# Kernel tuning notes

Hardware: AMD Instinct MI355X
Metric: run time of the kernel (lower is better)

## Reference

```python
import jax, jax.numpy as jnp
import numpy as np


def _bilinear(x, py, px):
    # x: [B,C,H,W]; py,px: [B,K,Ho,Wo] fractional sample coords (zero pad outside)
    B, C, H, W = x.shape
    K, Ho, Wo = py.shape[1], py.shape[2], py.shape[3]
    xf = x.reshape(B, C, H * W)
    y0 = jnp.floor(py)
    x0 = jnp.floor(px)

    def gather(yi, xi):
        valid = (yi >= 0) & (yi <= H - 1) & (xi >= 0) & (xi <= W - 1)
        yc = jnp.clip(yi, 0, H - 1).astype(jnp.int32)
        xc = jnp.clip(xi, 0, W - 1).astype(jnp.int32)
        idx = (yc * W + xc).reshape(B, 1, -1)  # [B,1,K*Ho*Wo]
        v = jnp.take_along_axis(xf, idx, axis=2)  # [B,C,K*Ho*Wo]
        return v * valid.reshape(B, 1, -1)

    wy1 = (py - y0).reshape(B, 1, -1)
    wx1 = (px - x0).reshape(B, 1, -1)
    wy0 = 1.0 - wy1
    wx0 = 1.0 - wx1
    v = (gather(y0, x0) * (wy0 * wx0)
         + gather(y0, x0 + 1) * (wy0 * wx1)
         + gather(y0 + 1, x0) * (wy1 * wx0)
         + gather(y0 + 1, x0 + 1) * (wy1 * wx1))
    return v.reshape(B, C, K, Ho, Wo)


def _deform_merge(x, w_off, b_off, w_def, gamma, beta):
    B, C, H, W = x.shape
    Co = w_def.shape[0]
    K, stride = 4, 2  # 2x2 kernel
    Ho, Wo = H // 2, W // 2
    # offset-predicting conv (same k/s/p as deform conv): [B, 2K, Ho, Wo]
    off = jax.lax.conv_general_dilated(x, w_off, (stride, stride), 'VALID')
    off = off + b_off[None, :, None, None]
    off = off.reshape(B, K, 2, Ho, Wo)  # (dy, dx) per kernel tap
    ky = jnp.arange(K) // 2
    kx = jnp.arange(K) % 2
    base_y = (jnp.arange(Ho) * stride)[None, None, :, None] + ky[None, :, None, None]
    base_x = (jnp.arange(Wo) * stride)[None, None, None, :] + kx[None, :, None, None]
    py = base_y.astype(x.dtype) + off[:, :, 0]
    px = base_x.astype(x.dtype) + off[:, :, 1]
    sampled = _bilinear(x, py, px)  # [B,C,K,Ho,Wo]
    y = jnp.einsum('bckhw,ock->bohw', sampled, w_def.reshape(Co, C, K))
    # BatchNorm2d (training-mode batch stats, eps=1e-5) + exact GELU
    mu = y.mean(axis=(0, 2, 3), keepdims=True)
    var = y.var(axis=(0, 2, 3), keepdims=True)
    yn = (y - mu) * jax.lax.rsqrt(var + 1e-5)
    yn = yn * gamma[None, :, None, None] + beta[None, :, None, None]
    yg = jax.nn.gelu(yn, approximate=False)
    return yg.reshape(B, Co, Ho * Wo).transpose(0, 2, 1)  # [B, L/4, Co]


def setup_inputs() -> dict:
    key = jax.random.key(0)
    k0, k1, k2 = jax.random.split(key, 3)
    B, C, H, W, Co = 16, 96, 112, 112, 192
    x = jax.random.normal(k0, (B, C, H, W), jnp.float32)
    # conv_offset: 2*kh*kw = 8 output channels (zero-init in mmcv; small random here)
    w_off = jax.random.normal(k1, (8, C, 2, 2), jnp.float32) * 0.01
    b_off = jnp.zeros((8,), jnp.float32)
    w_def = jax.random.normal(k2, (Co, C, 2, 2), jnp.float32) * (1.0 / np.sqrt(C * 4))
    gamma = jnp.ones((Co,), jnp.float32)
    beta = jnp.zeros((Co,), jnp.float32)
    return {"x": x, "h": H, "w": W, "w_off": w_off, "b_off": b_off,
            "w_def": w_def, "gamma": gamma, "beta": beta}


def reference(x, h, w, w_off, b_off, w_def, gamma, beta):
    assert x.shape[2] == h and x.shape[3] == w
    return _deform_merge(x, w_off, b_off, w_def, gamma, beta)
```

## Files before the change

### kernel.cpp

```cpp
#include <hip/hip_runtime.h>
#include <math.h>

#define BB 16
#define CC 96
#define HH 112
#define WW 112
#define HO 56
#define WO 56
#define LL (HO*WO)
#define CO 192
#define CKD 384
#define NPIX (BB*LL)

#define TPX 28
#define CHK 8
#define NCHUNK 12
#define WROWS 4
#define WCOLS 64
#define WSTRIDE 260
#define APAD 40

#define WS_SSUM  16
#define WS_SSQS  208
#define WS_B_OFF 4096
#define B_ELEMS  73728

typedef short bf16x8 __attribute__((ext_vector_type(8)));
typedef float f32x4  __attribute__((ext_vector_type(4)));

__device__ __forceinline__ void split8(const float4 a0, const float4 a1,
                                       bf16x8& hi, bf16x8& lo)
{
    float f[8] = {a0.x, a0.y, a0.z, a0.w, a1.x, a1.y, a1.z, a1.w};
    #pragma unroll
    for (int j = 0; j < 8; ++j) {
        unsigned bits = __float_as_uint(f[j]);
        float fh = __uint_as_float(bits & 0xFFFF0000u);
        float fl = f[j] - fh;
        hi[j] = (short)(bits >> 16);
        lo[j] = (short)(__float_as_uint(fl) >> 16);
    }
}

__global__ void k_zero(float* __restrict__ ws) {
    int t = threadIdx.x;
    if (t < 384) ws[WS_SSUM + t] = 0.f;
}

__global__ void k_prep(const float* __restrict__ w_def,
                       unsigned short* __restrict__ bhi,
                       unsigned short* __restrict__ blo,
                       float* __restrict__ ws)
{
    if (blockIdx.x == 0 && threadIdx.x < 384) ws[WS_SSUM + threadIdx.x] = 0.f;
    int t = blockIdx.x * 256 + threadIdx.x;
    if (t >= 12 * 12 * 64) return;
    int ln  = t & 63;
    int ks  = (t >> 6) % 12;
    int ntg = t / (64 * 12);
    int n  = ntg * 16 + (ln & 15);
    int k0 = ks * 32 + (ln >> 4) * 8;
    const float* wp = w_def + (size_t)n * CKD + k0;
    #pragma unroll
    for (int j = 0; j < 8; ++j) {
        float f = wp[j];
        unsigned bits = __float_as_uint(f);
        float fh = __uint_as_float(bits & 0xFFFF0000u);
        float fl = f - fh;
        bhi[t * 8 + j] = (unsigned short)(bits >> 16);
        blo[t * 8 + j] = (unsigned short)(__float_as_uint(fl) >> 16);
    }
}

template<bool PREP>
__device__ __forceinline__ void tile_body(
    const float* __restrict__ x, const float* __restrict__ w_off,
    const float* __restrict__ b_off, const float* __restrict__ w_def,
    const unsigned short* __restrict__ bhi, const unsigned short* __restrict__ blo,
    float* win, unsigned short* smAh, unsigned short* smAl, float* soff,
    int b, int bx, int tid, f32x4 (&acc)[2][3])
{
    const int oy  = bx >> 1;
    const int ox0 = (bx & 1) * TPX;
    const int iy  = oy * 2;
    const int ix0 = ox0 * 2;
    const int ln = tid & 63;
    const int w  = tid >> 6;

    float dacc = 0.f;
    const int cpix = tid >> 3;
    const int coch = tid & 7;
    const int spair = tid / 14;
    const int sq    = tid % 14;
    for (int ch = 0; ch < NCHUNK; ++ch) {
        __syncthreads();
        if (tid < 224) {
            int c = spair >> 1, r = spair & 1;
            const float* src = x + (((size_t)(b * CC + ch * CHK + c) * HH) + iy + r) * WW + ix0 + sq * 4;
            *(float4*)&win[(c * 2 + r) * 56 + sq * 4] = *(const float4*)src;
        }
        __syncthreads();
        if (tid < 224) {
            const float* wb = w_off + (size_t)coch * (CC * 4) + ch * CHK * 4;
            #pragma unroll
            for (int c = 0; c < CHK; ++c) {
                float2 t0 = *(const float2*)&win[(c * 2 + 0) * 56 + 2 * cpix];
                float2 t1 = *(const float2*)&win[(c * 2 + 1) * 56 + 2 * cpix];
                float4 a = *(const float4*)(wb + c * 4);
                dacc += t0.x * a.x + t0.y * a.y + t1.x * a.z + t1.y * a.w;
            }
        }
    }
    if (tid < 224) soff[cpix * 8 + coch] = dacc + b_off[coch];

    const int row0 = ln & 15;
    const int kg   = ln >> 4;
    const int skk = tid & 31;
    const int sc  = skk >> 2;
    const int sk  = skk & 3;
    const int sky = sk >> 1, skx = sk & 1;
    const int wr0 = iy - 1, wc0 = ix0 - 4;

    for (int ch = NCHUNK - 1; ch >= 0; --ch) {
        __syncthreads();
        #pragma unroll
        for (int j = 0; j < 2; ++j) {
            int li = tid + 256 * j;
            int cg = li & 15;
            int pr = li >> 4;
            int r = pr & 3, c = pr >> 2;
            int gr = min(max(wr0 + r, 0), HH - 1);
            int gc0 = wc0 + cg * 4;
            const float* src = x + (((size_t)(b * CC + ch * CHK + c) * HH) + gr) * WW;
            float4 v;
            if (gc0 >= 0 && gc0 <= WW - 4) {
                v = *(const float4*)(src + gc0);
            } else {
                v.x = src[min(max(gc0 + 0, 0), WW - 1)];
                v.y = src[min(max(gc0 + 1, 0), WW - 1)];
                v.z = src[min(max(gc0 + 2, 0), WW - 1)];
                v.w = src[min(max(gc0 + 3, 0), WW - 1)];
            }
            *(float4*)&win[c * WSTRIDE + r * WCOLS + cg * 4] = v;
        }
        __syncthreads();
        {
            const float* xc = x + ((size_t)(b * CC + ch * CHK + sc) * HH) * WW;
            const float* wchan = &win[sc * WSTRIDE];
            #pragma unroll
            for (int j = 0; j < 4; ++j) {
                if (j < 3 || tid < 128) {
                    int pix = (tid >> 5) + 8 * j;
                    float2 so = *(const float2*)&soff[pix * 8 + 2 * sk];
                    float fy = (float)(iy + sky) + so.x;
                    float fx = (float)(ix0 + 2 * pix + skx) + so.y;
                    float y0f = floorf(fy), x0f = floorf(fx);
                    int y0 = (int)y0f, x0 = (int)x0f;
                    float wy1 = fy - y0f, wx1 = fx - x0f;
                    float wy0 = 1.f - wy1, wx0 = 1.f - wx1;
                    int y1 = y0 + 1, x1 = x0 + 1;
                    bool vy0 = (y0 >= 0) && (y0 <= HH - 1);
                    bool vy1 = (y1 >= 0) && (y1 <= HH - 1);
                    bool vx0 = (x0 >= 0) && (x0 <= WW - 1);
                    bool vx1 = (x1 >= 0) && (x1 <= WW - 1);
                    int cy0 = min(max(y0, 0), HH - 1), cy1 = min(max(y1, 0), HH - 1);
                    int cx0 = min(max(x0, 0), WW - 1), cx1 = min(max(x1, 0), WW - 1);
                    float w00 = (vy0 && vx0) ? wy0 * wx0 : 0.f;
                    float w01 = (vy0 && vx1) ? wy0 * wx1 : 0.f;
                    float w10 = (vy1 && vx0) ? wy1 * wx0 : 0.f;
                    float w11 = (vy1 && vx1) ? wy1 * wx1 : 0.f;
                    int ry0 = cy0 - wr0, ry1 = cy1 - wr0;
                    int rx0 = cx0 - wc0, rx1 = cx1 - wc0;
                    bool inw = ((unsigned)ry0 <= (unsigned)(WROWS - 1)) &&
                               ((unsigned)ry1 <= (unsigned)(WROWS - 1)) &&
                               ((unsigned)rx0 <= (unsigned)(WCOLS - 1)) &&
                               ((unsigned)rx1 <= (unsigned)(WCOLS - 1));
                    float v;
                    if (inw) {
                        v = w00 * wchan[ry0 * WCOLS + rx0] + w01 * wchan[ry0 * WCOLS + rx1]
                          + w10 * wchan[ry1 * WCOLS + rx0] + w11 * wchan[ry1 * WCOLS + rx1];
                    } else {
                        v = w00 * xc[cy0 * WW + cx0] + w01 * xc[cy0 * WW + cx1]
                          + w10 * xc[cy1 * WW + cx0] + w11 * xc[cy1 * WW + cx1];
                    }
                    unsigned u = __float_as_uint(v);
                    float fh = __uint_as_float(u & 0xFFFF0000u);
                    smAh[pix * APAD + skk] = (unsigned short)(u >> 16);
                    smAl[pix * APAD + skk] = (unsigned short)(__float_as_uint(v - fh) >> 16);
                }
            }
        }
        __syncthreads();
        bf16x8 ah[2], al[2];
        #pragma unroll
        for (int mt = 0; mt < 2; ++mt) {
            ah[mt] = *(const bf16x8*)&smAh[(mt * 16 + row0) * APAD + kg * 8];
            al[mt] = *(const bf16x8*)&smAl[(mt * 16 + row0) * APAD + kg * 8];
        }
        #pragma unroll
        for (int nt = 0; nt < 3; ++nt) {
            bf16x8 bh, bl;
            if (PREP) {
                size_t idx = ((size_t)(((w * 3 + nt) * 12 + ch) * 64) + ln) * 8;
                bh = *(const bf16x8*)(bhi + idx);
                bl = *(const bf16x8*)(blo + idx);
            } else {
                const float* wp = w_def + (size_t)(w * 48 + nt * 16 + row0) * CKD
                                + ch * 32 + kg * 8;
                float4 b0 = *(const float4*)wp;
                float4 b1 = *(const float4*)(wp + 4);
                split8(b0, b1, bh, bl);
            }
            #pragma unroll
            for (int mt = 0; mt < 2; ++mt) {
                acc[mt][nt] = __builtin_amdgcn_mfma_f32_16x16x32_bf16(ah[mt], bh, acc[mt][nt], 0, 0, 0);
                acc[mt][nt] = __builtin_amdgcn_mfma_f32_16x16x32_bf16(ah[mt], bl, acc[mt][nt], 0, 0, 0);
                acc[mt][nt] = __builtin_amdgcn_mfma_f32_16x16x32_bf16(al[mt], bh, acc[mt][nt], 0, 0, 0);
            }
        }
    }
}

template<bool PREP>
__global__ __launch_bounds__(256, 6) void k_main(
    const float* __restrict__ x, const float* __restrict__ w_off,
    const float* __restrict__ b_off, const float* __restrict__ w_def,
    const unsigned short* __restrict__ bhi, const unsigned short* __restrict__ blo,
    float* __restrict__ yout, float* __restrict__ ws)
{
    __shared__ float win[CHK * WSTRIDE];
    __shared__ unsigned short smAh[32 * APAD];
    __shared__ unsigned short smAl[32 * APAD];
    __shared__ float soff[TPX * 8];

    const int tid = threadIdx.x;
    const int b  = blockIdx.y;
    const int bx = blockIdx.x;
    const int ln = tid & 63;
    const int w  = tid >> 6;
    const int row0 = ln & 15;
    const int kg   = ln >> 4;

    if (tid < 128) {
        int rr = 28 + (tid >> 5), cc = tid & 31;
        smAh[rr * APAD + cc] = 0;
        smAl[rr * APAD + cc] = 0;
    }

    f32x4 acc[2][3];
    #pragma unroll
    for (int mt = 0; mt < 2; ++mt)
        #pragma unroll
        for (int nt = 0; nt < 3; ++nt)
            acc[mt][nt] = (f32x4){0.f, 0.f, 0.f, 0.f};

    tile_body<PREP>(x, w_off, b_off, w_def, bhi, blo,
                    win, smAh, smAl, soff, b, bx, tid, acc);

    #pragma unroll
    for (int nt = 0; nt < 3; ++nt) {
        float s = 0.f, q = 0.f;
        #pragma unroll
        for (int mt = 0; mt < 2; ++mt)
            #pragma unroll
            for (int r = 0; r < 4; ++r) {
                float v = acc[mt][nt][r];
                s += v; q += v * v;
            }
        s += __shfl_xor(s, 16); s += __shfl_xor(s, 32);
        q += __shfl_xor(q, 16); q += __shfl_xor(q, 32);
        if (ln < 16) {
            atomicAdd(&ws[WS_SSUM + w * 48 + nt * 16 + ln], s);
            atomicAdd(&ws[WS_SSQS + w * 48 + nt * 16 + ln], q);
        }
    }
    int oy = bx >> 1, ox0 = (bx & 1) * TPX;
    size_t obase = (size_t)b * LL + (size_t)oy * WO + ox0;
    #pragma unroll
    for (int mt = 0; mt < 2; ++mt)
        #pragma unroll
        for (int r = 0; r < 4; ++r) {
            int pp = mt * 16 + kg * 4 + r;
            if (pp < TPX) {
                float* dst = yout + (obase + pp) * CO + w * 48 + row0;
                dst[0]  = acc[mt][0][r];
                dst[16] = acc[mt][1][r];
                dst[32] = acc[mt][2][r];
            }
        }
}

__global__ __launch_bounds__(256) void k_bn_gelu(
    float* __restrict__ out,
    const float* __restrict__ gamma,
    const float* __restrict__ beta,
    const float* __restrict__ ws)
{
    __shared__ float ssc[CO], ssh[CO];
    int t = threadIdx.x;
    if (t < CO) {
        float n = (float)NPIX;
        float mu = ws[WS_SSUM + t] / n;
        float var = ws[WS_SSQS + t] / n - mu * mu;
        float sc = gamma[t] * rsqrtf(fmaxf(var, 0.f) + 1e-5f);
        ssc[t] = sc;
        ssh[t] = beta[t] - mu * sc;
    }
    __syncthreads();
    long long i4 = ((long long)blockIdx.x * 256 + t) * 4;
    if (i4 >= (long long)NPIX * CO) return;
    int o0 = (int)(i4 % CO);
    float4* p = (float4*)(out + i4);
    float4 v = *p;
    float f[4] = { v.x, v.y, v.z, v.w };
    #pragma unroll
    for (int j = 0; j < 4; ++j) {
        float z = ssc[o0 + j] * f[j] + ssh[o0 + j];
        f[j] = 0.5f * z * (1.f + erff(z * 0.70710678118654752f));
    }
    v.x = f[0]; v.y = f[1]; v.z = f[2]; v.w = f[3];
    *p = v;
}

extern "C" void kernel_launch(void* const* d_in, const int* in_sizes, int n_in,
                              void* d_out, int out_size, void* d_ws, size_t ws_size,
                              hipStream_t stream)
{
    const float *x = nullptr, *w_off = nullptr, *b_off = nullptr;
    const float *w_def = nullptr, *gamma = nullptr, *beta = nullptr;
    for (int i = 0; i < n_in; ++i) {
        int s = in_sizes[i];
        if      (s == 19267584) x     = (const float*)d_in[i];
        else if (s == 3072)     w_off = (const float*)d_in[i];
        else if (s == 8)        b_off = (const float*)d_in[i];
        else if (s == 73728)    w_def = (const float*)d_in[i];
        else if (s == 192) { if (!gamma) gamma = (const float*)d_in[i];
                             else        beta  = (const float*)d_in[i]; }
    }
    if (!x || !w_off || !b_off || !w_def || !gamma || !beta) {
        x = (const float*)d_in[0]; w_off = (const float*)d_in[3];
        b_off = (const float*)d_in[4]; w_def = (const float*)d_in[5];
        gamma = (const float*)d_in[6]; beta = (const float*)d_in[7];
    }

    float* ws = (float*)d_ws;
    float* out = (float*)d_out;

    unsigned short* bhi = (unsigned short*)((char*)d_ws + WS_B_OFF);
    unsigned short* blo = bhi + B_ELEMS;
    bool prep = ws_size >= (size_t)(WS_B_OFF + 2 * B_ELEMS * sizeof(unsigned short));

    if (prep) {
        k_prep<<<36, 256, 0, stream>>>(w_def, bhi, blo, ws);
        k_main<true><<<dim3(112, BB), 256, 0, stream>>>(x, w_off, b_off, w_def, bhi, blo, out, ws);
    } else {
        k_zero<<<1, 384, 0, stream>>>(ws);
        k_main<false><<<dim3(112, BB), 256, 0, stream>>>(x, w_off, b_off, w_def, bhi, blo, out, ws);
    }
    k_bn_gelu<<<dim3((int)(((long long)NPIX*CO/4 + 255) / 256)), 256, 0, stream>>>(out, gamma, beta, ws);
}
```

Measured before the change: 368.5 us.

## Split offset conv into own kernel and use 512-thread main tiles

Moves the offset-predicting conv into a separate kernel that writes per-pixel offsets to workspace, computed per full output row. The main kernel then loads those offsets and runs with 512 threads, each wave owning one 16-row M tile, so staging and sampling work is spread over twice as many threads. This removes the serialized offset prologue from each main block and raises parallelism. In exchange it adds a launch and an offset round trip through global memory, and it depends on a larger workspace; the old path remains as a fallback and its occupancy hint was changed.

Result: faster. 336.5 us (-8.7%).

```diff
diff --git a/kernel.cpp b/kernel.cpp
--- a/kernel.cpp
+++ b/kernel.cpp
@@ -19,11 +19,14 @@
 #define WCOLS 64
 #define WSTRIDE 260
 #define APAD 40
+#define OSTRIDE 228
 
 #define WS_SSUM  16
 #define WS_SSQS  208
 #define WS_B_OFF 4096
 #define B_ELEMS  73728
+#define WS_SOFF_OFF 299008
+#define SOFF_BYTES (BB*HO*WO*8*4)
 
 typedef short bf16x8 __attribute__((ext_vector_type(8)));
 typedef float f32x4  __attribute__((ext_vector_type(4)));
@@ -72,66 +75,96 @@
     }
 }
 
-template<bool PREP>
-__device__ __forceinline__ void tile_body(
+__global__ __launch_bounds__(512) void k_off(
     const float* __restrict__ x, const float* __restrict__ w_off,
-    const float* __restrict__ b_off, const float* __restrict__ w_def,
+    const float* __restrict__ b_off, float* __restrict__ soff_all)
+{
+    __shared__ float win[CHK * OSTRIDE];
+    const int t  = threadIdx.x;
+    const int oy = blockIdx.x;
+    const int b  = blockIdx.y;
+    const int iy = oy * 2;
+    const int pix = t >> 3, och = t & 7;
+    float dacc = 0.f;
+    for (int ch = 0; ch < NCHUNK; ++ch) {
+        __syncthreads();
+        if (t < 448) {
+            int c = t / 56, u = t % 56;
+            int r = u / 28, q = u % 28;
+            const float* src = x + (((size_t)(b*CC + ch*CHK + c)*HH) + iy + r)*WW + q*4;
+            *(float4*)&win[c*OSTRIDE + r*112 + q*4] = *(const float4*)src;
+        }
+        __syncthreads();
+        if (t < 448) {
+            const float* wb = w_off + (size_t)och * (CC*4) + ch*CHK*4;
+            #pragma unroll
+            for (int c = 0; c < CHK; ++c) {
+                float2 t0 = *(const float2*)&win[c*OSTRIDE + 2*pix];
+                float2 t1 = *(const float2*)&win[c*OSTRIDE + 112 + 2*pix];
+                float4 a = *(const float4*)(wb + c*4);
+                dacc += t0.x*a.x + t0.y*a.y + t1.x*a.z + t1.y*a.w;
+            }
+        }
+    }
+    if (t < 448)
+        soff_all[((size_t)(b*HO + oy)*WO)*8 + t] = dacc + b_off[och];
+}
+
+__global__ __launch_bounds__(512, 8) void k_main8(
+    const float* __restrict__ x,
     const unsigned short* __restrict__ bhi, const unsigned short* __restrict__ blo,
-    float* win, unsigned short* smAh, unsigned short* smAl, float* soff,
-    int b, int bx, int tid, f32x4 (&acc)[2][3])
-{
+    const float* __restrict__ soff_all,
+    float* __restrict__ yout, float* __restrict__ ws)
+{
+    __shared__ float win[CHK * WSTRIDE];
+    __shared__ unsigned short smAh[32 * APAD];
+    __shared__ unsigned short smAl[32 * APAD];
+    __shared__ float soff[TPX * 8];
+
+    const int tid = threadIdx.x;
+    const int b  = blockIdx.y;
+    const int bx = blockIdx.x;
     const int oy  = bx >> 1;
     const int ox0 = (bx & 1) * TPX;
     const int iy  = oy * 2;
     const int ix0 = ox0 * 2;
     const int ln = tid & 63;
     const int w  = tid >> 6;
-
-    float dacc = 0.f;
-    const int cpix = tid >> 3;
-    const int coch = tid & 7;
-    const int spair = tid / 14;
-    const int sq    = tid % 14;
-    for (int ch = 0; ch < NCHUNK; ++ch) {
-        __syncthreads();
-        if (tid < 224) {
-            int c = spair >> 1, r = spair & 1;
-            const float* src = x + (((size_t)(b * CC + ch * CHK + c) * HH) + iy + r) * WW + ix0 + sq * 4;
-            *(float4*)&win[(c * 2 + r) * 56 + sq * 4] = *(const float4*)src;
-        }
-        __syncthreads();
-        if (tid < 224) {
-            const float* wb = w_off + (size_t)coch * (CC * 4) + ch * CHK * 4;
-            #pragma unroll
-            for (int c = 0; c < CHK; ++c) {
-                float2 t0 = *(const float2*)&win[(c * 2 + 0) * 56 + 2 * cpix];
-                float2 t1 = *(const float2*)&win[(c * 2 + 1) * 56 + 2 * cpix];
-                float4 a = *(const float4*)(wb + c * 4);
-                dacc += t0.x * a.x + t0.y * a.y + t1.x * a.z + t1.y * a.w;
-            }
-        }
-    }
-    if (tid < 224) soff[cpix * 8 + coch] = dacc + b_off[coch];
-
+    const int wr = w & 1;
+    const int wc = w >> 1;
     const int row0 = ln & 15;
     const int kg   = ln >> 4;
+
+    if (tid < 128) {
+        int rr = 28 + (tid >> 5), cc = tid & 31;
+        smAh[rr*APAD + cc] = 0;
+        smAl[rr*APAD + cc] = 0;
+    }
+    if (tid < 56) {
+        const float* sp = soff_all + ((size_t)(b*HO + oy)*WO + ox0)*8;
+        *(float4*)&soff[tid*4] = *(const float4*)(sp + tid*4);
+    }
+
+    const int cg  = tid & 15;
+    const int pr  = tid >> 4;
+    const int sr  = pr & 3;
+    const int scn = pr >> 2;
     const int skk = tid & 31;
     const int sc  = skk >> 2;
     const int sk  = skk & 3;
     const int sky = sk >> 1, skx = sk & 1;
     const int wr0 = iy - 1, wc0 = ix0 - 4;
 
+    f32x4 acc[3];
+    #pragma unroll
+    for (int nt = 0; nt < 3; ++nt) acc[nt] = (f32x4){0.f, 0.f, 0.f, 0.f};
+
     for (int ch = NCHUNK - 1; ch >= 0; --ch) {
         __syncthreads();
-        #pragma unroll
-        for (int j = 0; j < 2; ++j) {
-            int li = tid + 256 * j;
-            int cg = li & 15;
-            int pr = li >> 4;
-            int r = pr & 3, c = pr >> 2;
-            int gr = min(max(wr0 + r, 0), HH - 1);
+        {
+            int gr = min(max(wr0 + sr, 0), HH - 1);
             int gc0 = wc0 + cg * 4;
-            const float* src = x + (((size_t)(b * CC + ch * CHK + c) * HH) + gr) * WW;
+            const float* src = x + (((size_t)(b*CC + ch*CHK + scn)*HH) + gr)*WW;
             float4 v;
             if (gc0 >= 0 && gc0 <= WW - 4) {
                 v = *(const float4*)(src + gc0);
@@ -141,19 +174,19 @@
                 v.z = src[min(max(gc0 + 2, 0), WW - 1)];
                 v.w = src[min(max(gc0 + 3, 0), WW - 1)];
             }
-            *(float4*)&win[c * WSTRIDE + r * WCOLS + cg * 4] = v;
+            *(float4*)&win[scn*WSTRIDE + sr*WCOLS + cg*4] = v;
         }
         __syncthreads();
         {
-            const float* xc = x + ((size_t)(b * CC + ch * CHK + sc) * HH) * WW;
-            const float* wchan = &win[sc * WSTRIDE];
+            const float* xc = x + ((size_t)(b*CC + ch*CHK + sc)*HH)*WW;
+            const float* wchan = &win[sc*WSTRIDE];
             #pragma unroll
-            for (int j = 0; j < 4; ++j) {
-                if (j < 3 || tid < 128) {
-                    int pix = (tid >> 5) + 8 * j;
-                    float2 so = *(const float2*)&soff[pix * 8 + 2 * sk];
+            for (int j = 0; j < 2; ++j) {
+                int pix = (tid >> 5) + 16 * j;
+                if (pix < TPX) {
+                    float2 so = *(const float2*)&soff[pix*8 + 2*sk];
                     float fy = (float)(iy + sky) + so.x;
-                    float fx = (float)(ix0 + 2 * pix + skx) + so.y;
+                    float fx = (float)(ix0 + 2*pix + skx) + so.y;
                     float y0f = floorf(fy), x0f = floorf(fx);
                     int y0 = (int)y0f, x0 = (int)x0f;
                     float wy1 = fy - y0f, wx1 = fx - x0f;
@@ -177,36 +210,195 @@
                                ((unsigned)rx1 <= (unsigned)(WCOLS - 1));
                     float v;
                     if (inw) {
-                        v = w00 * wchan[ry0 * WCOLS + rx0] + w01 * wchan[ry0 * WCOLS + rx1]
-                          + w10 * wchan[ry1 * WCOLS + rx0] + w11 * wchan[ry1 * WCOLS + rx1];
+                        v = w00 * wchan[ry0*WCOLS + rx0] + w01 * wchan[ry0*WCOLS + rx1]
+                          + w10 * wchan[ry1*WCOLS + rx0] + w11 * wchan[ry1*WCOLS + rx1];
                     } else {
-                        v = w00 * xc[cy0 * WW + cx0] + w01 * xc[cy0 * WW + cx1]
-                          + w10 * xc[cy1 * WW + cx0] + w11 * xc[cy1 * WW + cx1];
+                        v = w00 * xc[cy0*WW + cx0] + w01 * xc[cy0*WW + cx1]
+                          + w10 * xc[cy1*WW + cx0] + w11 * xc[cy1*WW + cx1];
                     }
                     unsigned u = __float_as_uint(v);
                     float fh = __uint_as_float(u & 0xFFFF0000u);
-                    smAh[pix * APAD + skk] = (unsigned short)(u >> 16);
-                    smAl[pix * APAD + skk] = (unsigned short)(__float_as_uint(v - fh) >> 16);
+                    smAh[pix*APAD + skk] = (unsigned short)(u >> 16);
+                    smAl[pix*APAD + skk] = (unsigned short)(__float_as_uint(v - fh) >> 16);
                 }
             }
         }
         __syncthreads();
+        bf16x8 ah = *(const bf16x8*)&smAh[(wr*16 + row0)*APAD + kg*8];
+        bf16x8 al = *(const bf16x8*)&smAl[(wr*16 + row0)*APAD + kg*8];
+        #pragma unroll
+        for (int nt = 0; nt < 3; ++nt) {
+            size_t idx = ((size_t)(((wc*3 + nt)*12 + ch)*64) + ln)*8;
+            bf16x8 bh = *(const bf16x8*)(bhi + idx);
+            bf16x8 bl = *(const bf16x8*)(blo + idx);
+            acc[nt] = __builtin_amdgcn_mfma_f32_16x16x32_bf16(ah, bh, acc[nt], 0, 0, 0);
+            acc[nt] = __builtin_amdgcn_mfma_f32_16x16x32_bf16(ah, bl, acc[nt], 0, 0, 0);
+            acc[nt] = __builtin_amdgcn_mfma_f32_16x16x32_bf16(al, bh, acc[nt], 0, 0, 0);
+        }
+    }
+
+    #pragma unroll
+    for (int nt = 0; nt < 3; ++nt) {
+        float s = 0.f, q = 0.f;
+        #pragma unroll
+        for (int r = 0; r < 4; ++r) {
+            float v = acc[nt][r];
+            s += v; q += v * v;
+        }
+        s += __shfl_xor(s, 16); s += __shfl_xor(s, 32);
+        q += __shfl_xor(q, 16); q += __shfl_xor(q, 32);
+        if (ln < 16) {
+            atomicAdd(&ws[WS_SSUM + wc*48 + nt*16 + ln], s);
+            atomicAdd(&ws[WS_SSQS + wc*48 + nt*16 + ln], q);
+        }
+    }
+    size_t obase = (size_t)b * LL + (size_t)oy * WO + ox0;
+    #pragma unroll
+    for (int r = 0; r < 4; ++r) {
+        int pp = wr*16 + kg*4 + r;
+        if (pp < TPX) {
+            float* dst = yout + (obase + pp)*CO + wc*48 + row0;
+            dst[0]  = acc[0][r];
+            dst[16] = acc[1][r];
+            dst[32] = acc[2][r];
+        }
+    }
+}
+
+template<bool PREP>
+__device__ __forceinline__ void tile_body(
+    const float* __restrict__ x, const float* __restrict__ w_off,
+    const float* __restrict__ b_off, const float* __restrict__ w_def,
+    const unsigned short* __restrict__ bhi, const unsigned short* __restrict__ blo,
+    float* win, unsigned short* smAh, unsigned short* smAl, float* soff,
+    int b, int bx, int tid, f32x4 (&acc)[2][3])
+{
+    const int oy  = bx >> 1;
+    const int ox0 = (bx & 1) * TPX;
+    const int iy  = oy * 2;
+    const int ix0 = ox0 * 2;
+    const int ln = tid & 63;
+    const int w  = tid >> 6;
+
+    float dacc = 0.f;
+    const int cpix = tid >> 3;
+    const int coch = tid & 7;
+    const int spair = tid / 14;
+    const int sq    = tid % 14;
+    for (int ch = 0; ch < NCHUNK; ++ch) {
+        __syncthreads();
+        if (tid < 224) {
+            int c = spair >> 1, r = spair & 1;
+            const float* src = x + (((size_t)(b*CC + ch*CHK + c)*HH) + iy + r)*WW + ix0 + sq*4;
+            *(float4*)&win[(c*2 + r)*56 + sq*4] = *(const float4*)src;
+        }
+        __syncthreads();
+        if (tid < 224) {
+            const float* wb = w_off + (size_t)coch*(CC*4) + ch*CHK*4;
+            #pragma unroll
+            for (int c = 0; c < CHK; ++c) {
+                float2 t0 = *(const float2*)&win[(c*2 + 0)*56 + 2*cpix];
+                float2 t1 = *(const float2*)&win[(c*2 + 1)*56 + 2*cpix];
+                float4 a = *(const float4*)(wb + c*4);
+                dacc += t0.x*a.x + t0.y*a.y + t1.x*a.z + t1.y*a.w;
+            }
+        }
+    }
+    if (tid < 224) soff[cpix*8 + coch] = dacc + b_off[coch];
+
+    const int row0 = ln & 15;
+    const int kg   = ln >> 4;
+    const int skk = tid & 31;
+    const int sc  = skk >> 2;
+    const int sk  = skk & 3;
+    const int sky = sk >> 1, skx = sk & 1;
+    const int wr0 = iy - 1, wc0 = ix0 - 4;
+
+    for (int ch = NCHUNK - 1; ch >= 0; --ch) {
+        __syncthreads();
+        #pragma unroll
+        for (int j = 0; j < 2; ++j) {
+            int li = tid + 256*j;
+            int cg = li & 15;
+            int pr = li >> 4;
+            int r = pr & 3, c = pr >> 2;
+            int gr = min(max(wr0 + r, 0), HH - 1);
+            int gc0 = wc0 + cg*4;
+            const float* src = x + (((size_t)(b*CC + ch*CHK + c)*HH) + gr)*WW;
+            float4 v;
+            if (gc0 >= 0 && gc0 <= WW - 4) {
+                v = *(const float4*)(src + gc0);
+            } else {
+                v.x = src[min(max(gc0 + 0, 0), WW - 1)];
+                v.y = src[min(max(gc0 + 1, 0), WW - 1)];
+                v.z = src[min(max(gc0 + 2, 0), WW - 1)];
+                v.w = src[min(max(gc0 + 3, 0), WW - 1)];
+            }
+            *(float4*)&win[c*WSTRIDE + r*WCOLS + cg*4] = v;
+        }
+        __syncthreads();
+        {
+            const float* xc = x + ((size_t)(b*CC + ch*CHK + sc)*HH)*WW;
+            const float* wchan = &win[sc*WSTRIDE];
+            #pragma unroll
+            for (int j = 0; j < 4; ++j) {
+                if (j < 3 || tid < 128) {
+                    int pix = (tid >> 5) + 8*j;
+                    float2 so = *(const float2*)&soff[pix*8 + 2*sk];
+                    float fy = (float)(iy + sky) + so.x;
+                    float fx = (float)(ix0 + 2*pix + skx) + so.y;
+                    float y0f = floorf(fy), x0f = floorf(fx);
+                    int y0 = (int)y0f, x0 = (int)x0f;
+                    float wy1 = fy - y0f, wx1 = fx - x0f;
+                    float wy0 = 1.f - wy1, wx0 = 1.f - wx1;
+                    int y1 = y0 + 1, x1 = x0 + 1;
+                    bool vy0 = (y0 >= 0) && (y0 <= HH - 1);
+                    bool vy1 = (y1 >= 0) && (y1 <= HH - 1);
+                    bool vx0 = (x0 >= 0) && (x0 <= WW - 1);
+                    bool vx1 = (x1 >= 0) && (x1 <= WW - 1);
+                    int cy0 = min(max(y0, 0), HH - 1), cy1 = min(max(y1, 0), HH - 1);
+                    int cx0 = min(max(x0, 0), WW - 1), cx1 = min(max(x1, 0), WW - 1);
+                    float w00 = (vy0 && vx0) ? wy0*wx0 : 0.f;
+                    float w01 = (vy0 && vx1) ? wy0*wx1 : 0.f;
+                    float w10 = (vy1 && vx0) ? wy1*wx0 : 0.f;
+                    float w11 = (vy1 && vx1) ? wy1*wx1 : 0.f;
+                    int ry0 = cy0 - wr0, ry1 = cy1 - wr0;
+                    int rx0 = cx0 - wc0, rx1 = cx1 - wc0;
+                    bool inw = ((unsigned)ry0 <= (unsigned)(WROWS - 1)) &&
+                               ((unsigned)ry1 <= (unsigned)(WROWS - 1)) &&
+                               ((unsigned)rx0 <= (unsigned)(WCOLS - 1)) &&
+                               ((unsigned)rx1 <= (unsigned)(WCOLS - 1));
+                    float v;
+                    if (inw) {
+                        v = w00*wchan[ry0*WCOLS + rx0] + w01*wchan[ry0*WCOLS + rx1]
+                          + w10*wchan[ry1*WCOLS + rx0] + w11*wchan[ry1*WCOLS + rx1];
+                    } else {
+                        v = w00*xc[cy0*WW + cx0] + w01*xc[cy0*WW + cx1]
+                          + w10*xc[cy1*WW + cx0] + w11*xc[cy1*WW + cx1];
+                    }
+                    unsigned u = __float_as_uint(v);
+                    float fh = __uint_as_float(u & 0xFFFF0000u);
+                    smAh[pix*APAD + skk] = (unsigned short)(u >> 16);
+                    smAl[pix*APAD + skk] = (unsigned short)(__float_as_uint(v - fh) >> 16);
+                }
+            }
+        }
+        __syncthreads();
         bf16x8 ah[2], al[2];
         #pragma unroll
         for (int mt = 0; mt < 2; ++mt) {
-            ah[mt] = *(const bf16x8*)&smAh[(mt * 16 + row0) * APAD + kg * 8];
-            al[mt] = *(const bf16x8*)&smAl[(mt * 16 + row0) * APAD + kg * 8];
+            ah[mt] = *(const bf16x8*)&smAh[(mt*16 + row0)*APAD + kg*8];
+            al[mt] = *(const bf16x8*)&smAl[(mt*16 + row0)*APAD + kg*8];
         }
         #pragma unroll
         for (int nt = 0; nt < 3; ++nt) {
             bf16x8 bh, bl;
             if (PREP) {
-                size_t idx = ((size_t)(((w * 3 + nt) * 12 + ch) * 64) + ln) * 8;
+                size_t idx = ((size_t)(((w*3 + nt)*12 + ch)*64) + ln)*8;
                 bh = *(const bf16x8*)(bhi + idx);
                 bl = *(const bf16x8*)(blo + idx);
             } else {
-                const float* wp = w_def + (size_t)(w * 48 + nt * 16 + row0) * CKD
-                                + ch * 32 + kg * 8;
+                const float* wp = w_def + (size_t)(w*48 + nt*16 + row0)*CKD + ch*32 + kg*8;
                 float4 b0 = *(const float4*)wp;
                 float4 b1 = *(const float4*)(wp + 4);
                 split8(b0, b1, bh, bl);
@@ -222,7 +414,7 @@
 }
 
 template<bool PREP>
-__global__ __launch_bounds__(256, 6) void k_main(
+__global__ __launch_bounds__(256, 4) void k_main_r3(
     const float* __restrict__ x, const float* __restrict__ w_off,
     const float* __restrict__ b_off, const float* __restrict__ w_def,
     const unsigned short* __restrict__ bhi, const unsigned short* __restrict__ blo,
@@ -243,8 +435,8 @@
 
     if (tid < 128) {
         int rr = 28 + (tid >> 5), cc = tid & 31;
-        smAh[rr * APAD + cc] = 0;
-        smAl[rr * APAD + cc] = 0;
+        smAh[rr*APAD + cc] = 0;
+        smAl[rr*APAD + cc] = 0;
     }
 
     f32x4 acc[2][3];
@@ -270,19 +462,19 @@
         s += __shfl_xor(s, 16); s += __shfl_xor(s, 32);
         q += __shfl_xor(q, 16); q += __shfl_xor(q, 32);
         if (ln < 16) {
-            atomicAdd(&ws[WS_SSUM + w * 48 + nt * 16 + ln], s);
-            atomicAdd(&ws[WS_SSQS + w * 48 + nt * 16 + ln], q);
-        }
-    }
-    int oy = bx >> 1, ox0 = (bx & 1) * TPX;
-    size_t obase = (size_t)b * LL + (size_t)oy * WO + ox0;
+            atomicAdd(&ws[WS_SSUM + w*48 + nt*16 + ln], s);
+            atomicAdd(&ws[WS_SSQS + w*48 + nt*16 + ln], q);
+        }
+    }
+    int oy = bx >> 1, ox0 = (bx & 1)*TPX;
+    size_t obase = (size_t)b*LL + (size_t)oy*WO + ox0;
     #pragma unroll
     for (int mt = 0; mt < 2; ++mt)
         #pragma unroll
         for (int r = 0; r < 4; ++r) {
-            int pp = mt * 16 + kg * 4 + r;
+            int pp = mt*16 + kg*4 + r;
             if (pp < TPX) {
-                float* dst = yout + (obase + pp) * CO + w * 48 + row0;
+                float* dst = yout + (obase + pp)*CO + w*48 + row0;
                 dst[0]  = acc[mt][0][r];
                 dst[16] = acc[mt][1][r];
                 dst[32] = acc[mt][2][r];
@@ -348,14 +540,22 @@
 
     unsigned short* bhi = (unsigned short*)((char*)d_ws + WS_B_OFF);
     unsigned short* blo = bhi + B_ELEMS;
-    bool prep = ws_size >= (size_t)(WS_B_OFF + 2 * B_ELEMS * sizeof(unsigned short));
-
-    if (prep) {
+    float* soff_all = (float*)((char*)d_ws + WS_SOFF_OFF);
+    bool big = ws_size >= (size_t)(WS_SOFF_OFF + SOFF_BYTES);
+
+    if (big) {
         k_prep<<<36, 256, 0, stream>>>(w_def, bhi, blo, ws);
-        k_main<true><<<dim3(112, BB), 256, 0, stream>>>(x, w_off, b_off, w_def, bhi, blo, out, ws);
+        k_off<<<dim3(HO, BB), 512, 0, stream>>>(x, w_off, b_off, soff_all);
+        k_main8<<<dim3(112, BB), 512, 0, stream>>>(x, bhi, blo, soff_all, out, ws);
     } else {
-        k_zero<<<1, 384, 0, stream>>>(ws);
-        k_main<false><<<dim3(112, BB), 256, 0, stream>>>(x, w_off, b_off, w_def, bhi, blo, out, ws);
+        bool prep = ws_size >= (size_t)(WS_B_OFF + 2*B_ELEMS*sizeof(unsigned short));
+        if (prep) {
+            k_prep<<<36, 256, 0, stream>>>(w_def, bhi, blo, ws);
+            k_main_r3<true><<<dim3(112, BB), 256, 0, stream>>>(x, w_off, b_off, w_def, bhi, blo, out, ws);
+        } else {
+            k_zero<<<1, 384, 0, stream>>>(ws);
+            k_main_r3<false><<<dim3(112, BB), 256, 0, stream>>>(x, w_off, b_off, w_def, bhi, blo, out, ws);
+        }
     }
     k_bn_gelu<<<dim3((int)(((long long)NPIX*CO/4 + 255) / 256)), 256, 0, stream>>>(out, gamma, beta, ws);
 }
```
